# Kernel optimization log

Measured on AMD Instinct MI355X. Metric: run time of the kernel, lower is better.

The kernel has to match this reference:

```python
import jax, jax.numpy as jnp
import numpy as np

D_INSTR, D_ACT, D_OBJ, TOK = 768, 7, 256, 256


def setup_inputs() -> dict:
    key = jax.random.key(0)
    ks = jax.random.split(key, 10)
    B, NDEMO, NOBJ = 256, 16, 64
    inp = {
        "instr_embedding": jax.random.normal(ks[0], (B, D_INSTR), jnp.float32),
        "demo_object_embeddings": jax.random.normal(ks[1], (NDEMO, B, NOBJ, D_OBJ), jnp.float32),
        "demo_actions": jax.random.normal(ks[2], (NDEMO, B, D_ACT), jnp.float32),
        "current_object_embeddings": jax.random.normal(ks[3], (B, NOBJ, D_OBJ), jnp.float32),
        # learned params (stored as (in, out); equivalent math to torch Linear)
        "W_instr": jax.random.normal(ks[4], (D_INSTR, TOK), jnp.float32) / np.sqrt(D_INSTR),
        "b_instr": jax.random.normal(ks[5], (TOK,), jnp.float32) * 0.01,
        "W_act": jax.random.normal(ks[6], (D_ACT, TOK), jnp.float32) / np.sqrt(D_ACT),
        "b_act": jax.random.normal(ks[7], (TOK,), jnp.float32) * 0.01,
        "W_obj": jax.random.normal(ks[8], (D_OBJ, TOK), jnp.float32) / np.sqrt(D_OBJ),
        "b_obj": jax.random.normal(ks[9], (TOK,), jnp.float32) * 0.01,
    }
    return inp


def reference(instr_embedding, demo_object_embeddings, demo_actions,
              current_object_embeddings, W_instr, b_instr, W_act, b_act,
              W_obj, b_obj):
    # Project everything in single batched GEMMs (structure is uniform across batch,
    # so the per-example Python loop in the original collapses to dense ops).
    instr_tok = instr_embedding @ W_instr + b_instr            # (B, T)
    demo_obj_tok = jnp.einsum('dbnf,ft->dbnt', demo_object_embeddings, W_obj) + b_obj  # (D,B,No,T)
    act_tok = jnp.einsum('dbf,ft->dbt', demo_actions, W_act) + b_act                   # (D,B,T)
    cur_tok = jnp.einsum('bnf,ft->bnt', current_object_embeddings, W_obj) + b_obj      # (B,No,T)

    D, B, No, T = demo_obj_tok.shape
    # Per demo: [objects..., action] -> (D, B, No+1, T), then interleave demos in order.
    demo_block = jnp.concatenate([demo_obj_tok, act_tok[:, :, None, :]], axis=2)
    demo_block = demo_block.transpose(1, 0, 2, 3).reshape(B, D * (No + 1), T)
    # Final sequence: [instr, demo1_objs, demo1_action, ..., current_objs]
    return jnp.concatenate([instr_tok[:, None, :], demo_block, cur_tok], axis=1)
```

## Files before the change

kernel.cpp:

```cpp
#include <hip/hip_runtime.h>
#include <hip/hip_bf16.h>
#include <stdint.h>

#define TOK   256
#define NOBJ  64
#define NDEMO 16
#define BATCH 256
#define SEQ   1105
#define NDG   (NDEMO * BATCH)
#define NGRP  (NDG + BATCH)
#define NHT   (NGRP * 2)
#define NG    8
#define OBJ_BLKS   (NHT / NG)
#define ACT_BLKS   512
#define INSTR_BLKS 128
#define TOTAL_BLKS (ACT_BLKS + INSTR_BLKS + OBJ_BLKS)

typedef __bf16 bf16x8 __attribute__((ext_vector_type(8)));
typedef float  f32x4  __attribute__((ext_vector_type(4)));

static __device__ __forceinline__ unsigned pack_bf16x2(float a, float b) {
    unsigned ua = __float_as_uint(a);
    unsigned ub = __float_as_uint(b);
    unsigned ra = (ua + 0x7FFFu + ((ua >> 16) & 1u)) >> 16;
    unsigned rb = (ub + 0x7FFFu + ((ub >> 16) & 1u)) >> 16;
    return (ra & 0xFFFFu) | (rb << 16);
}

static __device__ __forceinline__ void gload_lds16(const float* g, void* l) {
    __builtin_amdgcn_global_load_lds(
        (const __attribute__((address_space(1))) uint32_t*)g,
        (__attribute__((address_space(3))) uint32_t*)l,
        16, 0, 0);
}

__global__ void wconv_frag_kernel(const float* __restrict__ W, uint16_t* __restrict__ Wf) {
    int q = blockIdx.x * 256 + threadIdx.x;
    int lane = q & 63;
    int s  = (q >> 6) & 7;
    int j  = (q >> 9) & 3;
    int wc = (q >> 11) & 3;
    int tcol = wc * 64 + j * 16 + (lane & 15);
    int k0   = s * 32 + (lane >> 4) * 8;
    uint4 w;
    unsigned p[4];
#pragma unroll
    for (int h = 0; h < 4; ++h) {
        float a = W[(size_t)(k0 + 2 * h)     * TOK + tcol];
        float b = W[(size_t)(k0 + 2 * h + 1) * TOK + tcol];
        p[h] = pack_bf16x2(a, b);
    }
    w.x = p[0]; w.y = p[1]; w.z = p[2]; w.w = p[3];
    *reinterpret_cast<uint4*>(Wf + (size_t)q * 8) = w;
}

__global__ __launch_bounds__(256, 2) void fused_kernel(
    const float* __restrict__ demo_obj,
    const float* __restrict__ cur,
    const float* __restrict__ b_obj,
    const __bf16* __restrict__ Wf,
    const float* __restrict__ demo_act,
    const float* __restrict__ W_act,
    const float* __restrict__ b_act,
    const float* __restrict__ instr,
    const float* __restrict__ W_instr,
    const float* __restrict__ b_instr,
    float* __restrict__ out)
{
    __shared__ __align__(16) unsigned char lds_raw[65536];
    float* F = reinterpret_cast<float*>(lds_raw);
    int blk = blockIdx.x;
    int tid = threadIdx.x;

    if (blk >= ACT_BLKS + INSTR_BLKS) {
        int ob = blk - (ACT_BLKS + INSTR_BLKS);
        int h0 = ob * NG;
        const float* base = (h0 < 2 * NDG)
            ? demo_obj + (size_t)h0 * (32 * TOK)
            : cur + (size_t)(h0 - 2 * NDG) * (32 * TOK);

        int wave = tid >> 6, lane = tid & 63;
        int l15 = lane & 15, l4 = lane >> 4;
        int n0 = wave * 64;

        auto STAGE = [&](int it) {
            const float* sb = base + (size_t)it * (32 * TOK);
#pragma unroll
            for (int i = 0; i < 8; ++i)
                gload_lds16(sb + (size_t)(i * 256 + tid) * 4,
                            F + (size_t)(i * 256 + tid) * 4);
        };

        bf16x8 wf[4][8];
        {
            const __bf16* fb = Wf + ((size_t)wave * 32 * 64 + lane) * 8;
#pragma unroll
            for (int j = 0; j < 4; ++j)
#pragma unroll
                for (int s = 0; s < 8; ++s)
                    wf[j][s] = *reinterpret_cast<const bf16x8*>(fb + (size_t)(j * 8 + s) * 64 * 8);
        }
#pragma unroll
        for (int j = 0; j < 4; ++j)
#pragma unroll
            for (int s = 0; s < 8; ++s)
                asm volatile("" : "+v"(wf[j][s]));

        f32x4 bv4[4];
#pragma unroll
        for (int j = 0; j < 4; ++j) {
            bv4[j] = *reinterpret_cast<const f32x4*>(b_obj + n0 + j * 16 + l4 * 4);
            asm volatile("" : "+v"(bv4[j]));
        }

        STAGE(0);

#pragma unroll 1
        for (int it = 0; it < NG; ++it) {
            if (it == 0) asm volatile("s_waitcnt vmcnt(0)" ::: "memory");
            else         asm volatile("s_waitcnt vmcnt(8)" ::: "memory");
            __builtin_amdgcn_s_barrier();
            __builtin_amdgcn_sched_barrier(0);

            __bf16* B = reinterpret_cast<__bf16*>(lds_raw + 32768 + (it & 1) * 16384);
#pragma unroll
            for (int i = 0; i < 4; ++i) {
                int p = i * 256 + tid;
                int row = p >> 5;
                int c8  = p & 31;
                float4 lo = *reinterpret_cast<const float4*>(F + (size_t)p * 8);
                float4 hi = *reinterpret_cast<const float4*>(F + (size_t)p * 8 + 4);
                bf16x8 o;
                o[0] = (__bf16)lo.x; o[1] = (__bf16)lo.y;
                o[2] = (__bf16)lo.z; o[3] = (__bf16)lo.w;
                o[4] = (__bf16)hi.x; o[5] = (__bf16)hi.y;
                o[6] = (__bf16)hi.z; o[7] = (__bf16)hi.w;
                unsigned off = (unsigned)(row * 512 + c8 * 16) ^ (unsigned)((row & 7) << 4);
                *reinterpret_cast<bf16x8*>(reinterpret_cast<unsigned char*>(B) + off) = o;
            }
            asm volatile("s_waitcnt lgkmcnt(0)" ::: "memory");
            __builtin_amdgcn_sched_barrier(0);
            __builtin_amdgcn_s_barrier();
            __builtin_amdgcn_sched_barrier(0);

            if (it + 1 < NG) STAGE(it + 1);

            const unsigned char* Bb = lds_raw + 32768 + (it & 1) * 16384;
            f32x4 acc[2][4];
#pragma unroll
            for (int i = 0; i < 2; ++i)
#pragma unroll
                for (int j = 0; j < 4; ++j) {
                    f32x4 z = {0.0f, 0.0f, 0.0f, 0.0f};
                    acc[i][j] = z;
                }

#pragma unroll
            for (int s = 0; s < 8; ++s) {
                bf16x8 a[2];
#pragma unroll
                for (int i = 0; i < 2; ++i) {
                    int r = i * 16 + l15;
                    unsigned off = (unsigned)(r * 512 + s * 64 + l4 * 16) ^ (unsigned)((r & 7) << 4);
                    a[i] = *reinterpret_cast<const bf16x8*>(Bb + off);
                }
#pragma unroll
                for (int j = 0; j < 4; ++j) {
                    acc[0][j] = __builtin_amdgcn_mfma_f32_16x16x32_bf16(wf[j][s], a[0], acc[0][j], 0, 0, 0);
                    acc[1][j] = __builtin_amdgcn_mfma_f32_16x16x32_bf16(wf[j][s], a[1], acc[1][j], 0, 0, 0);
                }
            }

            int h = h0 + it;
            int gg = h >> 1, half = h & 1;
            int row_base;
            if (h < 2 * NDG) {
                int d = gg >> 8, b = gg & 255;
                row_base = b * SEQ + 1 + d * (NOBJ + 1) + half * 32;
            } else {
                int b = gg - NDG;
                row_base = b * SEQ + 1 + NDEMO * (NOBJ + 1) + half * 32;
            }
#pragma unroll
            for (int i = 0; i < 2; ++i) {
                int row = row_base + i * 16 + l15;
#pragma unroll
                for (int j = 0; j < 4; ++j) {
                    f32x4 v = acc[i][j] + bv4[j];
                    *reinterpret_cast<f32x4*>(out + (size_t)row * TOK + n0 + j * 16 + l4 * 4) = v;
                }
            }
        }

    } else if (blk < ACT_BLKS) {
        int g8 = blk * 8;
        int t = tid;
        float v[8];
        float bb = b_act[t];
#pragma unroll
        for (int r = 0; r < 8; ++r) v[r] = bb;
#pragma unroll
        for (int k = 0; k < 7; ++k) {
            float wv = W_act[k * TOK + t];
#pragma unroll
            for (int r = 0; r < 8; ++r)
                v[r] += demo_act[(size_t)(g8 + r) * 7 + k] * wv;
        }
#pragma unroll
        for (int r = 0; r < 8; ++r) {
            int g = g8 + r;
            int d = g >> 8, b = g & 255;
            out[(size_t)(b * SEQ + (d + 1) * (NOBJ + 1)) * TOK + t] = v[r];
        }

    } else {
        int b0 = (blk - ACT_BLKS) * 2;
        int t = tid;
        float* buf = F;
        const float* src = instr + (size_t)b0 * 768;
#pragma unroll
        for (int i = 0; i < 6; ++i) buf[i * 256 + t] = src[i * 256 + t];
        __syncthreads();
        float a0 = b_instr[t], a1 = a0;
#pragma unroll 4
        for (int k = 0; k < 768; ++k) {
            float wv = W_instr[(size_t)k * TOK + t];
            a0 += buf[k] * wv;
            a1 += buf[768 + k] * wv;
        }
        out[(size_t)b0 * SEQ * TOK + t] = a0;
        out[(size_t)(b0 + 1) * SEQ * TOK + t] = a1;
    }
}

extern "C" void kernel_launch(void* const* d_in, const int* in_sizes, int n_in,
                              void* d_out, int out_size, void* d_ws, size_t ws_size,
                              hipStream_t stream) {
    (void)in_sizes; (void)n_in; (void)out_size; (void)ws_size;
    const float* instr    = (const float*)d_in[0];
    const float* demo_obj = (const float*)d_in[1];
    const float* demo_act = (const float*)d_in[2];
    const float* cur      = (const float*)d_in[3];
    const float* W_instr  = (const float*)d_in[4];
    const float* b_instr  = (const float*)d_in[5];
    const float* W_act    = (const float*)d_in[6];
    const float* b_act    = (const float*)d_in[7];
    const float* W_obj    = (const float*)d_in[8];
    const float* b_obj    = (const float*)d_in[9];
    float* out = (float*)d_out;

    uint16_t* Wf = (uint16_t*)d_ws;

    wconv_frag_kernel<<<32, 256, 0, stream>>>(W_obj, Wf);
    fused_kernel<<<TOTAL_BLKS, 256, 0, stream>>>(
        demo_obj, cur, b_obj, (const __bf16*)d_ws,
        demo_act, W_act, b_act, instr, W_instr, b_instr, out);
}
```

Baseline: 157.2 us.

## Add dedicated producer wave for object staging and read fp32 directly from LDS

```diff
diff --git a/kernel.cpp b/kernel.cpp
--- a/kernel.cpp
+++ b/kernel.cpp
@@ -14,7 +14,7 @@
 #define OBJ_BLKS   (NHT / NG)
 #define ACT_BLKS   512
 #define INSTR_BLKS 128
-#define TOTAL_BLKS (ACT_BLKS + INSTR_BLKS + OBJ_BLKS)
+#define TOTAL_BLKS (OBJ_BLKS + ACT_BLKS + INSTR_BLKS)
 
 typedef __bf16 bf16x8 __attribute__((ext_vector_type(8)));
 typedef float  f32x4  __attribute__((ext_vector_type(4)));
@@ -25,6 +25,15 @@
     unsigned ra = (ua + 0x7FFFu + ((ua >> 16) & 1u)) >> 16;
     unsigned rb = (ub + 0x7FFFu + ((ub >> 16) & 1u)) >> 16;
     return (ra & 0xFFFFu) | (rb << 16);
+}
+
+static __device__ __forceinline__ bf16x8 pack8n(float4 lo, float4 hi) {
+    bf16x8 o;
+    o[0] = (__bf16)lo.x; o[1] = (__bf16)lo.y;
+    o[2] = (__bf16)lo.z; o[3] = (__bf16)lo.w;
+    o[4] = (__bf16)hi.x; o[5] = (__bf16)hi.y;
+    o[6] = (__bf16)hi.z; o[7] = (__bf16)hi.w;
+    return o;
 }
 
 static __device__ __forceinline__ void gload_lds16(const float* g, void* l) {
@@ -54,7 +63,7 @@
     *reinterpret_cast<uint4*>(Wf + (size_t)q * 8) = w;
 }
 
-__global__ __launch_bounds__(256, 2) void fused_kernel(
+__global__ __launch_bounds__(320, 2) void fused_kernel(
     const float* __restrict__ demo_obj,
     const float* __restrict__ cur,
     const float* __restrict__ b_obj,
@@ -67,169 +76,172 @@
     const float* __restrict__ b_instr,
     float* __restrict__ out)
 {
-    __shared__ __align__(16) unsigned char lds_raw[65536];
-    float* F = reinterpret_cast<float*>(lds_raw);
+    __shared__ __align__(16) float F[2][32 * TOK];
     int blk = blockIdx.x;
     int tid = threadIdx.x;
 
-    if (blk >= ACT_BLKS + INSTR_BLKS) {
-        int ob = blk - (ACT_BLKS + INSTR_BLKS);
+    if (blk < OBJ_BLKS) {
+        int ob = (blk & 7) * (OBJ_BLKS / 8) + (blk >> 3);
         int h0 = ob * NG;
         const float* base = (h0 < 2 * NDG)
             ? demo_obj + (size_t)h0 * (32 * TOK)
             : cur + (size_t)(h0 - 2 * NDG) * (32 * TOK);
 
         int wave = tid >> 6, lane = tid & 63;
-        int l15 = lane & 15, l4 = lane >> 4;
-        int n0 = wave * 64;
-
-        auto STAGE = [&](int it) {
-            const float* sb = base + (size_t)it * (32 * TOK);
-#pragma unroll
-            for (int i = 0; i < 8; ++i)
-                gload_lds16(sb + (size_t)(i * 256 + tid) * 4,
-                            F + (size_t)(i * 256 + tid) * 4);
-        };
-
-        bf16x8 wf[4][8];
-        {
-            const __bf16* fb = Wf + ((size_t)wave * 32 * 64 + lane) * 8;
+
+        if (wave == 4) {
+            auto STAGE = [&](int it) {
+                const float* sb = base + (size_t)it * (32 * TOK);
+                float* dst = &F[it & 1][0];
+#pragma unroll
+                for (int i = 0; i < 32; ++i) {
+                    gload_lds16(sb + (size_t)(i * 64 + (lane ^ (i & 7))) * 4,
+                                dst + (size_t)(i * 64 + lane) * 4);
+                }
+            };
+            STAGE(0);
+#pragma unroll 1
+            for (int it = 0; it < NG; ++it) {
+                __builtin_amdgcn_s_barrier();
+                __builtin_amdgcn_sched_barrier(0);
+                if (it + 1 < NG) {
+                    STAGE(it + 1);
+                    asm volatile("s_waitcnt vmcnt(32)" ::: "memory");
+                } else {
+                    asm volatile("s_waitcnt vmcnt(0)" ::: "memory");
+                }
+                __builtin_amdgcn_sched_barrier(0);
+                __builtin_amdgcn_s_barrier();
+                __builtin_amdgcn_sched_barrier(0);
+            }
+        } else {
+            int l15 = lane & 15, l4 = lane >> 4;
+            int n0 = wave * 64;
+
+            bf16x8 wf[4][8];
+            {
+                const __bf16* fb = Wf + ((size_t)wave * 32 * 64 + lane) * 8;
+#pragma unroll
+                for (int j = 0; j < 4; ++j)
+#pragma unroll
+                    for (int s = 0; s < 8; ++s)
+                        wf[j][s] = *reinterpret_cast<const bf16x8*>(fb + (size_t)(j * 8 + s) * 64 * 8);
+            }
 #pragma unroll
             for (int j = 0; j < 4; ++j)
 #pragma unroll
                 for (int s = 0; s < 8; ++s)
-                    wf[j][s] = *reinterpret_cast<const bf16x8*>(fb + (size_t)(j * 8 + s) * 64 * 8);
-        }
-#pragma unroll
-        for (int j = 0; j < 4; ++j)
-#pragma unroll
-            for (int s = 0; s < 8; ++s)
-                asm volatile("" : "+v"(wf[j][s]));
-
-        f32x4 bv4[4];
-#pragma unroll
-        for (int j = 0; j < 4; ++j) {
-            bv4[j] = *reinterpret_cast<const f32x4*>(b_obj + n0 + j * 16 + l4 * 4);
-            asm volatile("" : "+v"(bv4[j]));
-        }
-
-        STAGE(0);
+                    asm volatile("" : "+v"(wf[j][s]));
+
+            f32x4 bv4[4];
+#pragma unroll
+            for (int j = 0; j < 4; ++j) {
+                bv4[j] = *reinterpret_cast<const f32x4*>(b_obj + n0 + j * 16 + l4 * 4);
+                asm volatile("" : "+v"(bv4[j]));
+            }
 
 #pragma unroll 1
-        for (int it = 0; it < NG; ++it) {
-            if (it == 0) asm volatile("s_waitcnt vmcnt(0)" ::: "memory");
-            else         asm volatile("s_waitcnt vmcnt(8)" ::: "memory");
-            __builtin_amdgcn_s_barrier();
-            __builtin_amdgcn_sched_barrier(0);
-
-            __bf16* B = reinterpret_cast<__bf16*>(lds_raw + 32768 + (it & 1) * 16384);
-#pragma unroll
-            for (int i = 0; i < 4; ++i) {
-                int p = i * 256 + tid;
-                int row = p >> 5;
-                int c8  = p & 31;
-                float4 lo = *reinterpret_cast<const float4*>(F + (size_t)p * 8);
-                float4 hi = *reinterpret_cast<const float4*>(F + (size_t)p * 8 + 4);
-                bf16x8 o;
-                o[0] = (__bf16)lo.x; o[1] = (__bf16)lo.y;
-                o[2] = (__bf16)lo.z; o[3] = (__bf16)lo.w;
-                o[4] = (__bf16)hi.x; o[5] = (__bf16)hi.y;
-                o[6] = (__bf16)hi.z; o[7] = (__bf16)hi.w;
-                unsigned off = (unsigned)(row * 512 + c8 * 16) ^ (unsigned)((row & 7) << 4);
-                *reinterpret_cast<bf16x8*>(reinterpret_cast<unsigned char*>(B) + off) = o;
-            }
-            asm volatile("s_waitcnt lgkmcnt(0)" ::: "memory");
-            __builtin_amdgcn_sched_barrier(0);
-            __builtin_amdgcn_s_barrier();
-            __builtin_amdgcn_sched_barrier(0);
-
-            if (it + 1 < NG) STAGE(it + 1);
-
-            const unsigned char* Bb = lds_raw + 32768 + (it & 1) * 16384;
-            f32x4 acc[2][4];
-#pragma unroll
-            for (int i = 0; i < 2; ++i)
-#pragma unroll
-                for (int j = 0; j < 4; ++j) {
-                    f32x4 z = {0.0f, 0.0f, 0.0f, 0.0f};
-                    acc[i][j] = z;
-                }
-
-#pragma unroll
-            for (int s = 0; s < 8; ++s) {
-                bf16x8 a[2];
+            for (int it = 0; it < NG; ++it) {
+                __builtin_amdgcn_s_barrier();
+                __builtin_amdgcn_s_barrier();
+                __builtin_amdgcn_sched_barrier(0);
+
+                const float* buf = &F[it & 1][0];
+                f32x4 acc[2][4];
+#pragma unroll
+                for (int i = 0; i < 2; ++i)
+#pragma unroll
+                    for (int j = 0; j < 4; ++j) {
+                        f32x4 z = {0.0f, 0.0f, 0.0f, 0.0f};
+                        acc[i][j] = z;
+                    }
+
+#pragma unroll
+                for (int s = 0; s < 8; ++s) {
+                    bf16x8 a[2];
+#pragma unroll
+                    for (int i = 0; i < 2; ++i) {
+                        int r = i * 16 + l15;
+                        int c0 = s * 8 + l4 * 2;
+                        float4 lo = *reinterpret_cast<const float4*>(
+                            buf + r * TOK + (size_t)((c0 ^ (r & 7)) * 4));
+                        float4 hi = *reinterpret_cast<const float4*>(
+                            buf + r * TOK + (size_t)(((c0 + 1) ^ (r & 7)) * 4));
+                        a[i] = pack8n(lo, hi);
+                    }
+#pragma unroll
+                    for (int j = 0; j < 4; ++j) {
+                        acc[0][j] = __builtin_amdgcn_mfma_f32_16x16x32_bf16(wf[j][s], a[0], acc[0][j], 0, 0, 0);
+                        acc[1][j] = __builtin_amdgcn_mfma_f32_16x16x32_bf16(wf[j][s], a[1], acc[1][j], 0, 0, 0);
+                    }
+                }
+
+                int h = h0 + it;
+                int gg = h >> 1, half = h & 1;
+                int row_base;
+                if (h < 2 * NDG) {
+                    int d = gg >> 8, b = gg & 255;
+                    row_base = b * SEQ + 1 + d * (NOBJ + 1) + half * 32;
+                } else {
+                    int b = gg - NDG;
+                    row_base = b * SEQ + 1 + NDEMO * (NOBJ + 1) + half * 32;
+                }
 #pragma unroll
                 for (int i = 0; i < 2; ++i) {
-                    int r = i * 16 + l15;
-                    unsigned off = (unsigned)(r * 512 + s * 64 + l4 * 16) ^ (unsigned)((r & 7) << 4);
-                    a[i] = *reinterpret_cast<const bf16x8*>(Bb + off);
-                }
-#pragma unroll
-                for (int j = 0; j < 4; ++j) {
-                    acc[0][j] = __builtin_amdgcn_mfma_f32_16x16x32_bf16(wf[j][s], a[0], acc[0][j], 0, 0, 0);
-                    acc[1][j] = __builtin_amdgcn_mfma_f32_16x16x32_bf16(wf[j][s], a[1], acc[1][j], 0, 0, 0);
-                }
-            }
-
-            int h = h0 + it;
-            int gg = h >> 1, half = h & 1;
-            int row_base;
-            if (h < 2 * NDG) {
-                int d = gg >> 8, b = gg & 255;
-                row_base = b * SEQ + 1 + d * (NOBJ + 1) + half * 32;
-            } else {
-                int b = gg - NDG;
-                row_base = b * SEQ + 1 + NDEMO * (NOBJ + 1) + half * 32;
-            }
-#pragma unroll
-            for (int i = 0; i < 2; ++i) {
-                int row = row_base + i * 16 + l15;
-#pragma unroll
-                for (int j = 0; j < 4; ++j) {
-                    f32x4 v = acc[i][j] + bv4[j];
-                    *reinterpret_cast<f32x4*>(out + (size_t)row * TOK + n0 + j * 16 + l4 * 4) = v;
-                }
-            }
-        }
-
-    } else if (blk < ACT_BLKS) {
-        int g8 = blk * 8;
+                    int row = row_base + i * 16 + l15;
+#pragma unroll
+                    for (int j = 0; j < 4; ++j) {
+                        f32x4 v = acc[i][j] + bv4[j];
+                        *reinterpret_cast<f32x4*>(out + (size_t)row * TOK + n0 + j * 16 + l4 * 4) = v;
+                    }
+                }
+            }
+        }
+
+    } else if (blk < OBJ_BLKS + ACT_BLKS) {
+        if (tid < 256) {
+            int g8 = (blk - OBJ_BLKS) * 8;
+            int t = tid;
+            float v[8];
+            float bb = b_act[t];
+#pragma unroll
+            for (int r = 0; r < 8; ++r) v[r] = bb;
+#pragma unroll
+            for (int k = 0; k < 7; ++k) {
+                float wv = W_act[k * TOK + t];
+#pragma unroll
+                for (int r = 0; r < 8; ++r)
+                    v[r] += demo_act[(size_t)(g8 + r) * 7 + k] * wv;
+            }
+#pragma unroll
+            for (int r = 0; r < 8; ++r) {
+                int g = g8 + r;
+                int d = g >> 8, b = g & 255;
+                out[(size_t)(b * SEQ + (d + 1) * (NOBJ + 1)) * TOK + t] = v[r];
+            }
+        }
+
+    } else {
+        int b0 = (blk - OBJ_BLKS - ACT_BLKS) * 2;
         int t = tid;
-        float v[8];
-        float bb = b_act[t];
-#pragma unroll
-        for (int r = 0; r < 8; ++r) v[r] = bb;
-#pragma unroll
-        for (int k = 0; k < 7; ++k) {
-            float wv = W_act[k * TOK + t];
-#pragma unroll
-            for (int r = 0; r < 8; ++r)
-                v[r] += demo_act[(size_t)(g8 + r) * 7 + k] * wv;
-        }
-#pragma unroll
-        for (int r = 0; r < 8; ++r) {
-            int g = g8 + r;
-            int d = g >> 8, b = g & 255;
-            out[(size_t)(b * SEQ + (d + 1) * (NOBJ + 1)) * TOK + t] = v[r];
-        }
-
-    } else {
-        int b0 = (blk - ACT_BLKS) * 2;
-        int t = tid;
-        float* buf = F;
+        float* buf = &F[0][0];
         const float* src = instr + (size_t)b0 * 768;
-#pragma unroll
-        for (int i = 0; i < 6; ++i) buf[i * 256 + t] = src[i * 256 + t];
+        if (t < 256) {
+#pragma unroll
+            for (int i = 0; i < 6; ++i) buf[i * 256 + t] = src[i * 256 + t];
+        }
         __syncthreads();
-        float a0 = b_instr[t], a1 = a0;
+        if (t < 256) {
+            float a0 = b_instr[t], a1 = a0;
 #pragma unroll 4
-        for (int k = 0; k < 768; ++k) {
-            float wv = W_instr[(size_t)k * TOK + t];
-            a0 += buf[k] * wv;
-            a1 += buf[768 + k] * wv;
-        }
-        out[(size_t)b0 * SEQ * TOK + t] = a0;
-        out[(size_t)(b0 + 1) * SEQ * TOK + t] = a1;
+            for (int k = 0; k < 768; ++k) {
+                float wv = W_instr[(size_t)k * TOK + t];
+                a0 += buf[k] * wv;
+                a1 += buf[768 + k] * wv;
+            }
+            out[(size_t)b0 * SEQ * TOK + t] = a0;
+            out[(size_t)(b0 + 1) * SEQ * TOK + t] = a1;
+        }
     }
 }
 
@@ -252,7 +264,7 @@
     uint16_t* Wf = (uint16_t*)d_ws;
 
     wconv_frag_kernel<<<32, 256, 0, stream>>>(W_obj, Wf);
-    fused_kernel<<<TOTAL_BLKS, 256, 0, stream>>>(
+    fused_kernel<<<TOTAL_BLKS, 320, 0, stream>>>(
         demo_obj, cur, b_obj, (const __bf16*)d_ws,
         demo_act, W_act, b_act, instr, W_instr, b_instr, out);
 }
```

Measured after the change: 204.9 us. 30.3% more time.
